# Optimization experiments

Hardware: AMD Instinct MI355X
Metric: run time of the kernel (lower is better)

The kernel has to match this reference:

```python
import jax, jax.numpy as jnp
import numpy as np

B, N, C, H = 2, 384, 256, 4
D = C // H


def setup_inputs() -> dict:
    key = jax.random.key(0)
    k1, k2 = jax.random.split(key)
    x = jax.random.normal(k1, (B, N, C), dtype=jnp.float32)
    # nn.Linear(dim, 8*dim, bias=False) weight, scaled like default torch init magnitude
    W = jax.random.normal(k2, (8 * C, C), dtype=jnp.float32) / np.float32(np.sqrt(C))
    return {"x": x, "W": W}


def reference(x, W):
    Bx, Nx, Cx = x.shape
    Hh = H
    Dd = Cx // Hh
    scale = Dd ** -0.5
    # w(x): [B,N,8C] -> [B,N,8,H,D] -> [8,B,H,N,D]
    w = (x @ W.T).reshape(Bx, Nx, 8, Hh, Dd).transpose(2, 0, 3, 1, 4)
    a, b, c = w[0], w[1], w[2]          # w[3..5] (d,e,f) are unused in the torch forward
    v1, v2 = w[6], w[7]
    # pairwise logits, each [B,H,N,N]
    eAB = jnp.exp(jnp.einsum('bhid,bhjd->bhij', a, b) * scale)  # indexed [i,j]
    eCD = jnp.exp(jnp.einsum('bhid,bhjd->bhij', b, c) * scale)  # indexed [i,k]
    eEF = jnp.exp(jnp.einsum('bhid,bhjd->bhij', c, a) * scale)  # indexed [j,k]
    # exact factorization of exp(AB[ij]+CD[ik]+EF[jk]):
    # num[i,d] = sum_j eAB[ij] v1[jd] * (sum_k eCD[ik] eEF[jk] v2[kd])
    T = eEF[..., None] * v2[:, :, None, :, :]                   # [B,H,j,k,D]
    R = jnp.einsum('bhik,bhjkd->bhijd', eCD, T)                 # [B,H,i,j,D]
    num = jnp.einsum('bhij,bhjd,bhijd->bhid', eAB, v1, R)       # [B,H,N,D]
    den = jnp.sum(eAB * jnp.einsum('bhik,bhjk->bhij', eCD, eEF), axis=-1)  # [B,H,N]
    out = num / den[..., None]
    # [B,H,N,D] -> [B,N,H,D] -> [B,N,C]
    return out.transpose(0, 2, 1, 3).reshape(Bx, Nx, Cx)
```

## Files before the change

kernel.cpp:

```cpp
#include <hip/hip_runtime.h>
#include <math.h>

#define B_  2
#define N_  384
#define C_  256
#define H_  4
#define D_  64
#define NBH (B_*H_)
#define TSZ (NBH*N_*D_)
#define ESZ (NBH*N_*N_)
#define SCALE 0.125f
#define PIT 72

typedef _Float16 f16;
typedef f16  f16x8 __attribute__((ext_vector_type(8)));
typedef f16  f16x4 __attribute__((ext_vector_type(4)));
typedef float f32x4 __attribute__((ext_vector_type(4)));

__global__ __launch_bounds__(256) void proj_kernel(const float* __restrict__ x,
                                                   const float* __restrict__ W,
                                                   float* __restrict__ proj) {
    __shared__ float Xs[32][68];
    __shared__ float Ws[32][68];
    const int tid = threadIdx.x;
    const int tx = tid & 15, ty = tid >> 4;
    const int m0 = blockIdx.x * 64;
    const int c0 = blockIdx.y * 64;
    const int t  = c0 >> 8;
    const int wbase = ((t >= 3) ? (t + 3) : t) * 256;

    float acc[4][4] = {{0.f}};
    for (int k0 = 0; k0 < 256; k0 += 32) {
        __syncthreads();
#pragma unroll
        for (int l = 0; l < 8; ++l) {
            const int idx = l * 256 + tid;
            const int mi = idx >> 5, kk = idx & 31;
            Xs[kk][mi] = x[(m0 + mi) * 256 + k0 + kk];
            const int rem = (c0 + mi) & 255;
            Ws[kk][mi] = W[(wbase + rem) * 256 + k0 + kk];
        }
        __syncthreads();
#pragma unroll
        for (int kk = 0; kk < 32; ++kk) {
            const float4 xf = *(const float4*)&Xs[kk][ty * 4];
            const float4 wf = *(const float4*)&Ws[kk][tx * 4];
            const float xa[4] = {xf.x, xf.y, xf.z, xf.w};
            const float wa[4] = {wf.x, wf.y, wf.z, wf.w};
#pragma unroll
            for (int q = 0; q < 4; ++q)
#pragma unroll
                for (int p = 0; p < 4; ++p)
                    acc[q][p] += xa[q] * wa[p];
        }
    }
#pragma unroll
    for (int q = 0; q < 4; ++q) {
        const int r = m0 + ty * 4 + q;
        const int b = r / N_;
        const int n = r - b * N_;
#pragma unroll
        for (int p = 0; p < 4; ++p) {
            const int rem = (c0 + tx * 4 + p) & 255;
            const int h = rem >> 6, d = rem & 63;
            proj[t * TSZ + ((b * H_ + h) * N_ + n) * D_ + d] = acc[q][p];
        }
    }
}

__global__ __launch_bounds__(256) void logits_kernel(const float* __restrict__ proj,
                                                     f16* __restrict__ eabt16,
                                                     float* __restrict__ ecd,
                                                     f16* __restrict__ eef16) {
    __shared__ float Xs[32][68];
    __shared__ float Ys[32][68];
    const int tid = threadIdx.x;
    const int tx = tid & 15, ty = tid >> 4;
    const int i0 = blockIdx.x * 64, j0 = blockIdx.y * 64;
    const int q  = blockIdx.z >> 3;
    const int bh = blockIdx.z & 7;
    const int xt = q;
    const int yt = (q == 2) ? 0 : (q + 1);
    const float* Xp = proj + xt * TSZ + bh * N_ * D_;
    const float* Yp = proj + yt * TSZ + bh * N_ * D_;

    float acc[4][4] = {{0.f}};
    for (int k0 = 0; k0 < 64; k0 += 32) {
        __syncthreads();
#pragma unroll
        for (int l = 0; l < 8; ++l) {
            const int idx = l * 256 + tid;
            const int mi = idx >> 5, kk = idx & 31;
            Xs[kk][mi] = Xp[(i0 + mi) * 64 + k0 + kk];
            Ys[kk][mi] = Yp[(j0 + mi) * 64 + k0 + kk];
        }
        __syncthreads();
#pragma unroll
        for (int kk = 0; kk < 32; ++kk) {
            const float4 xf = *(const float4*)&Xs[kk][ty * 4];
            const float4 yf = *(const float4*)&Ys[kk][tx * 4];
            const float xa[4] = {xf.x, xf.y, xf.z, xf.w};
            const float ya[4] = {yf.x, yf.y, yf.z, yf.w};
#pragma unroll
            for (int qq = 0; qq < 4; ++qq)
#pragma unroll
                for (int p = 0; p < 4; ++p)
                    acc[qq][p] += xa[qq] * ya[p];
        }
    }
#pragma unroll
    for (int qq = 0; qq < 4; ++qq)
#pragma unroll
        for (int p = 0; p < 4; ++p) {
            const float e = expf(acc[qq][p] * SCALE);
            const int ii = i0 + ty * 4 + qq;
            const int jj = j0 + tx * 4 + p;
            if (q == 0)      eabt16[(size_t)bh * N_ * N_ + jj * N_ + ii] = (f16)e;
            else if (q == 1) ecd   [(size_t)bh * N_ * N_ + ii * N_ + jj] = e;
            else             eef16 [(size_t)bh * N_ * N_ + ii * N_ + jj] = (f16)e;
        }
}

__global__ __launch_bounds__(256) void triplet_mfma_kernel(
        const f16*  __restrict__ eabt,
        const float* __restrict__ ecd,
        const f16*  __restrict__ eef,
        const float* __restrict__ v1,
        const float* __restrict__ v2,
        float* __restrict__ numout) {
    __shared__ __align__(16) unsigned char smem_raw[62464];
    f16*   us   = (f16*)smem_raw;
    f16*   es   = us + 4 * 64 * PIT;
    f16*   abts = es + 64 * PIT;
    float* v1s  = (float*)(smem_raw + 55296);
    float* v2k  = (float*)(smem_raw + 61440);

    const int tid  = threadIdx.x;
    const int lane = tid & 63;
    const int w    = tid >> 6;
    const int quad = lane >> 4;
    const int lr   = lane & 15;
    const int i0 = blockIdx.x * 64;
    const int dg = blockIdx.y;
    const int bh = blockIdx.z;
    const int dd = dg * 4 + w;

    const f16*   eabtb = eabt + (size_t)bh * N_ * N_;
    const float* ecdb  = ecd  + (size_t)bh * N_ * N_;
    const f16*   eefb  = eef  + (size_t)bh * N_ * N_;
    const float* v1b   = v1 + (size_t)bh * N_ * D_;
    const float* v2b   = v2 + (size_t)bh * N_ * D_;

#pragma unroll
    for (int it = 0; it < 6; ++it) {
        const int id = it * 256 + tid;
        const int j = id >> 2, c = id & 3;
        const int d2 = dg * 4 + c;
        v1s[id] = (d2 < 64) ? v1b[j * 64 + d2] : 1.0f;
    }

    float numacc[16];
#pragma unroll
    for (int r = 0; r < 16; ++r) numacc[r] = 0.f;

    for (int kt = 0; kt < 6; ++kt) {
        const int k0 = kt * 64;
        __syncthreads();
        {
            const int c = tid >> 6, k = tid & 63;
            const int d2 = dg * 4 + c;
            v2k[c * 64 + k] = (d2 < 64) ? v2b[(k0 + k) * 64 + d2] : 1.0f;
        }
        __syncthreads();
#pragma unroll
        for (int it = 0; it < 4; ++it) {
            const int row  = it * 16 + (tid >> 4);
            const int kcol = (tid & 15) * 4;
            const float4 c4 = *(const float4*)&ecdb[(i0 + row) * N_ + k0 + kcol];
#pragma unroll
            for (int d = 0; d < 4; ++d) {
                const float4 w4 = *(const float4*)&v2k[d * 64 + kcol];
                union { f16 h[4]; unsigned long long u; } pk;
                pk.h[0] = (f16)(c4.x * w4.x);
                pk.h[1] = (f16)(c4.y * w4.y);
                pk.h[2] = (f16)(c4.z * w4.z);
                pk.h[3] = (f16)(c4.w * w4.w);
                *(unsigned long long*)(us + d * 64 * PIT + row * PIT + kcol) = pk.u;
            }
        }
        __syncthreads();
        f16x8 af[4][2];
#pragma unroll
        for (int isub = 0; isub < 4; ++isub)
#pragma unroll
            for (int ks = 0; ks < 2; ++ks)
                af[isub][ks] = *(const f16x8*)(us + w * 64 * PIT +
                                               (isub * 16 + lr) * PIT + (ks * 4 + quad) * 8);

        for (int jt = 0; jt < 6; ++jt) {
            const int j0 = jt * 64;
            __syncthreads();
#pragma unroll
            for (int it = 0; it < 2; ++it) {
                const int row = it * 32 + (tid >> 3);
                const int blk = tid & 7;
                *(uint4*)(es   + row * PIT + blk * 8) =
                    *(const uint4*)(eefb  + (j0 + row) * N_ + k0 + blk * 8);
                *(uint4*)(abts + row * PIT + blk * 8) =
                    *(const uint4*)(eabtb + (j0 + row) * N_ + i0 + blk * 8);
            }
            __syncthreads();
            f16x8 bf[4][2];
#pragma unroll
            for (int js = 0; js < 4; ++js)
#pragma unroll
                for (int ks = 0; ks < 2; ++ks)
                    bf[js][ks] = *(const f16x8*)(es + (js * 16 + lr) * PIT + (ks * 4 + quad) * 8);
#pragma unroll
            for (int js = 0; js < 4; ++js) {
                const float v1v = v1s[(j0 + js * 16 + lr) * 4 + w];
#pragma unroll
                for (int isub = 0; isub < 4; ++isub) {
                    f32x4 t = {0.f, 0.f, 0.f, 0.f};
                    t = __builtin_amdgcn_mfma_f32_16x16x32_f16(af[isub][0], bf[js][0], t, 0, 0, 0);
                    t = __builtin_amdgcn_mfma_f32_16x16x32_f16(af[isub][1], bf[js][1], t, 0, 0, 0);
                    const f16x4 ab = *(const f16x4*)(abts + (js * 16 + lr) * PIT +
                                                     isub * 16 + quad * 4);
#pragma unroll
                    for (int q = 0; q < 4; ++q)
                        numacc[isub * 4 + q] += (float)ab[q] * (v1v * t[q]);
                }
            }
        }
    }
#pragma unroll
    for (int r = 0; r < 16; ++r) {
        float v = numacc[r];
        v += __shfl_xor(v, 1);
        v += __shfl_xor(v, 2);
        v += __shfl_xor(v, 4);
        v += __shfl_xor(v, 8);
        numacc[r] = v;
    }
    if (lr == 0) {
#pragma unroll
        for (int r = 0; r < 16; ++r) {
            const int i = (r >> 2) * 16 + quad * 4 + (r & 3);
            numout[((size_t)bh * N_ + i0 + i) * 68 + dd] = numacc[r];
        }
    }
}

__global__ __launch_bounds__(256) void finalize_kernel(const float* __restrict__ numw,
                                                       float* __restrict__ out) {
    const int o = blockIdx.x * 256 + threadIdx.x;
    const int b = o / (N_ * C_);
    const int rem = o - b * (N_ * C_);
    const int n = rem >> 8;
    const int cc = rem & 255;
    const int h = cc >> 6, d = cc & 63;
    const float* base = numw + (((size_t)b * H_ + h) * N_ + n) * 68;
    out[o] = base[d] / base[64];
}

extern "C" void kernel_launch(void* const* d_in, const int* in_sizes, int n_in,
                              void* d_out, int out_size, void* d_ws, size_t ws_size,
                              hipStream_t stream) {
    const float* x = (const float*)d_in[0];
    const float* W = (const float*)d_in[1];
    float* ws    = (float*)d_ws;
    float* proj  = ws;
    float* ecd   = ws + 5 * TSZ;
    float* numw  = ecd + ESZ;
    f16*   eabt  = (f16*)(numw + NBH * N_ * 68);
    f16*   eef   = eabt + ESZ;

    proj_kernel<<<dim3(12, 20), 256, 0, stream>>>(x, W, proj);
    logits_kernel<<<dim3(6, 6, 24), 256, 0, stream>>>(proj, eabt, ecd, eef);
    triplet_mfma_kernel<<<dim3(6, 17, 8), 256, 0, stream>>>(
        eabt, ecd, eef, proj + 3 * TSZ, proj + 4 * TSZ, numw);
    finalize_kernel<<<dim3(768), 256, 0, stream>>>(numw, (float*)d_out);
}
```

Baseline: 252.2 us.

## Double triplet kernel block to 512 threads, splitting i rows across wave halves

The triplet MFMA kernel now runs 8 waves per block instead of 4. Each d-slot is handled by two waves that split the 64 i rows. This halves per-wave accumulators and A fragments, and B fragments are now loaded per js instead of held in registers. The aim is more waves in flight and lower register pressure for the same shared-memory tile. The cost is that the shared e/abt tile loads are repeated by more waves, along with extra synchronisation among more threads.

```diff
diff --git a/kernel.cpp b/kernel.cpp
--- a/kernel.cpp
+++ b/kernel.cpp
@@ -121,7 +121,7 @@
         }
 }
 
-__global__ __launch_bounds__(256) void triplet_mfma_kernel(
+__global__ __launch_bounds__(512) void triplet_mfma_kernel(
         const f16*  __restrict__ eabt,
         const float* __restrict__ ecd,
         const f16*  __restrict__ eef,
@@ -138,12 +138,14 @@
     const int tid  = threadIdx.x;
     const int lane = tid & 63;
     const int w    = tid >> 6;
+    const int ds   = w & 3;
+    const int ih   = w >> 2;
     const int quad = lane >> 4;
     const int lr   = lane & 15;
     const int i0 = blockIdx.x * 64;
     const int dg = blockIdx.y;
     const int bh = blockIdx.z;
-    const int dd = dg * 4 + w;
+    const int dd = dg * 4 + ds;
 
     const f16*   eabtb = eabt + (size_t)bh * N_ * N_;
     const float* ecdb  = ecd  + (size_t)bh * N_ * N_;
@@ -152,29 +154,31 @@
     const float* v2b   = v2 + (size_t)bh * N_ * D_;
 
 #pragma unroll
-    for (int it = 0; it < 6; ++it) {
-        const int id = it * 256 + tid;
+    for (int it = 0; it < 3; ++it) {
+        const int id = it * 512 + tid;
         const int j = id >> 2, c = id & 3;
         const int d2 = dg * 4 + c;
         v1s[id] = (d2 < 64) ? v1b[j * 64 + d2] : 1.0f;
     }
 
-    float numacc[16];
-#pragma unroll
-    for (int r = 0; r < 16; ++r) numacc[r] = 0.f;
+    float numacc[8];
+#pragma unroll
+    for (int r = 0; r < 8; ++r) numacc[r] = 0.f;
+
+    const f32x4 zero4 = {0.f, 0.f, 0.f, 0.f};
 
     for (int kt = 0; kt < 6; ++kt) {
         const int k0 = kt * 64;
         __syncthreads();
-        {
+        if (tid < 256) {
             const int c = tid >> 6, k = tid & 63;
             const int d2 = dg * 4 + c;
             v2k[c * 64 + k] = (d2 < 64) ? v2b[(k0 + k) * 64 + d2] : 1.0f;
         }
         __syncthreads();
 #pragma unroll
-        for (int it = 0; it < 4; ++it) {
-            const int row  = it * 16 + (tid >> 4);
+        for (int it = 0; it < 2; ++it) {
+            const int row  = it * 32 + (tid >> 4);
             const int kcol = (tid & 15) * 4;
             const float4 c4 = *(const float4*)&ecdb[(i0 + row) * N_ + k0 + kcol];
 #pragma unroll
@@ -189,20 +193,20 @@
             }
         }
         __syncthreads();
-        f16x8 af[4][2];
-#pragma unroll
-        for (int isub = 0; isub < 4; ++isub)
+        f16x8 af[2][2];
+#pragma unroll
+        for (int isub = 0; isub < 2; ++isub)
 #pragma unroll
             for (int ks = 0; ks < 2; ++ks)
-                af[isub][ks] = *(const f16x8*)(us + w * 64 * PIT +
-                                               (isub * 16 + lr) * PIT + (ks * 4 + quad) * 8);
+                af[isub][ks] = *(const f16x8*)(us + ds * 64 * PIT +
+                                               ((ih * 2 + isub) * 16 + lr) * PIT +
+                                               (ks * 4 + quad) * 8);
 
         for (int jt = 0; jt < 6; ++jt) {
             const int j0 = jt * 64;
             __syncthreads();
-#pragma unroll
-            for (int it = 0; it < 2; ++it) {
-                const int row = it * 32 + (tid >> 3);
+            {
+                const int row = tid >> 3;
                 const int blk = tid & 7;
                 *(uint4*)(es   + row * PIT + blk * 8) =
                     *(const uint4*)(eefb  + (j0 + row) * N_ + k0 + blk * 8);
@@ -210,22 +214,18 @@
                     *(const uint4*)(eabtb + (j0 + row) * N_ + i0 + blk * 8);
             }
             __syncthreads();
-            f16x8 bf[4][2];
-#pragma unroll
-            for (int js = 0; js < 4; ++js)
-#pragma unroll
-                for (int ks = 0; ks < 2; ++ks)
-                    bf[js][ks] = *(const f16x8*)(es + (js * 16 + lr) * PIT + (ks * 4 + quad) * 8);
 #pragma unroll
             for (int js = 0; js < 4; ++js) {
-                const float v1v = v1s[(j0 + js * 16 + lr) * 4 + w];
-#pragma unroll
-                for (int isub = 0; isub < 4; ++isub) {
-                    f32x4 t = {0.f, 0.f, 0.f, 0.f};
-                    t = __builtin_amdgcn_mfma_f32_16x16x32_f16(af[isub][0], bf[js][0], t, 0, 0, 0);
-                    t = __builtin_amdgcn_mfma_f32_16x16x32_f16(af[isub][1], bf[js][1], t, 0, 0, 0);
+                const f16x8 bf0 = *(const f16x8*)(es + (js * 16 + lr) * PIT + quad * 8);
+                const f16x8 bf1 = *(const f16x8*)(es + (js * 16 + lr) * PIT + (4 + quad) * 8);
+                const float v1v = v1s[(j0 + js * 16 + lr) * 4 + ds];
+#pragma unroll
+                for (int isub = 0; isub < 2; ++isub) {
+                    f32x4 t;
+                    t = __builtin_amdgcn_mfma_f32_16x16x32_f16(af[isub][0], bf0, zero4, 0, 0, 0);
+                    t = __builtin_amdgcn_mfma_f32_16x16x32_f16(af[isub][1], bf1, t, 0, 0, 0);
                     const f16x4 ab = *(const f16x4*)(abts + (js * 16 + lr) * PIT +
-                                                     isub * 16 + quad * 4);
+                                                     (ih * 2 + isub) * 16 + quad * 4);
 #pragma unroll
                     for (int q = 0; q < 4; ++q)
                         numacc[isub * 4 + q] += (float)ab[q] * (v1v * t[q]);
@@ -234,7 +234,7 @@
         }
     }
 #pragma unroll
-    for (int r = 0; r < 16; ++r) {
+    for (int r = 0; r < 8; ++r) {
         float v = numacc[r];
         v += __shfl_xor(v, 1);
         v += __shfl_xor(v, 2);
@@ -244,8 +244,8 @@
     }
     if (lr == 0) {
 #pragma unroll
-        for (int r = 0; r < 16; ++r) {
-            const int i = (r >> 2) * 16 + quad * 4 + (r & 3);
+        for (int r = 0; r < 8; ++r) {
+            const int i = (ih * 2 + (r >> 2)) * 16 + quad * 4 + (r & 3);
             numout[((size_t)bh * N_ + i0 + i) * 68 + dd] = numacc[r];
         }
     }
@@ -277,7 +277,7 @@
 
     proj_kernel<<<dim3(12, 20), 256, 0, stream>>>(x, W, proj);
     logits_kernel<<<dim3(6, 6, 24), 256, 0, stream>>>(proj, eabt, ecd, eef);
-    triplet_mfma_kernel<<<dim3(6, 17, 8), 256, 0, stream>>>(
+    triplet_mfma_kernel<<<dim3(6, 17, 8), 512, 0, stream>>>(
         eabt, ecd, eef, proj + 3 * TSZ, proj + 4 * TSZ, numw);
     finalize_kernel<<<dim3(768), 256, 0, stream>>>(numw, (float*)d_out);
 }
```

Result: slower. 270.4 us (+7.2%).
